# Kernel optimization log

Measured on AMD Instinct MI355X. Metric: run time of the kernel, lower is better.

## Reference

```python
import jax, jax.numpy as jnp
import numpy as np
import math

B, T, C = 4, 2048, 1024
NH = 16
HD = C // NH


def setup_inputs() -> dict:
    key = jax.random.key(0)
    ks = jax.random.split(key, 10)
    s = 0.02
    x = jax.random.normal(ks[0], (B, T, C), dtype=jnp.float32)
    W_qkv = jax.random.normal(ks[1], (C, 3 * C), dtype=jnp.float32) * s
    b_qkv = jnp.zeros((3 * C,), dtype=jnp.float32)
    W_proj = jax.random.normal(ks[2], (C, C), dtype=jnp.float32) * s
    b_proj = jnp.zeros((C,), dtype=jnp.float32)
    asym_mean, asym_std = 1.0, 0.7
    q_scale = jax.random.normal(ks[3], (NH, HD), dtype=jnp.float32) * asym_std + asym_mean
    q_bias = jax.random.normal(ks[4], (NH, HD), dtype=jnp.float32) * asym_std + asym_mean
    k_scale = jax.random.normal(ks[5], (NH, HD), dtype=jnp.float32) * asym_std + asym_mean
    k_bias = jax.random.normal(ks[6], (NH, HD), dtype=jnp.float32) * asym_std + asym_mean
    return {"x": x, "W_qkv": W_qkv, "b_qkv": b_qkv, "W_proj": W_proj,
            "b_proj": b_proj, "q_scale": q_scale, "q_bias": q_bias,
            "k_scale": k_scale, "k_bias": k_bias}


def reference(x, W_qkv, b_qkv, W_proj, b_proj, q_scale, q_bias, k_scale, k_bias):
    Bx, Tx, Cx = x.shape
    qkv = x @ W_qkv + b_qkv                       # [B,T,3C]
    q, k, v = jnp.split(qkv, 3, axis=-1)
    # [B,T,C] -> [B,NH,T,HD]
    reshape = lambda t: t.reshape(Bx, Tx, NH, HD).transpose(0, 2, 1, 3)
    q, k, v = reshape(q), reshape(k), reshape(v)
    # per-head affine scaling of Q/K
    q = q * q_scale[None, :, None, :] + q_bias[None, :, None, :]
    k = k * k_scale[None, :, None, :] + k_bias[None, :, None, :]
    scores = jnp.einsum('bhqd,bhkd->bhqk', q, k) / math.sqrt(HD)  # [B,NH,T,T]
    causal = jnp.tril(jnp.ones((Tx, Tx), dtype=bool))
    scores = jnp.where(causal[None, None], scores, -jnp.inf)
    att = jax.nn.softmax(scores, axis=-1)
    y = jnp.einsum('bhqk,bhkd->bhqd', att, v)     # [B,NH,T,HD]
    y = y.transpose(0, 2, 1, 3).reshape(Bx, Tx, Cx)
    return y @ W_proj + b_proj
```

## Files before the change

kernel.cpp:

```cpp
#include <hip/hip_runtime.h>
#include <hip/hip_bf16.h>

typedef unsigned short u16;
typedef __attribute__((ext_vector_type(8))) short short8;
typedef __attribute__((ext_vector_type(4))) float floatx4;

#define B_SZ 4
#define T_SZ 2048
#define C_SZ 1024
#define NH_SZ 16
#define HD_SZ 64
#define M_TOT 8192
#define K_DIM 1024

#define QSCALE 0.1803368801111204f

#define OFF_XB   ((size_t)16)
#define OFF_WQT  (OFF_XB + 8388608)
#define OFF_WPT  (OFF_WQT + 3145728)
#define OFF_PB   (OFF_WPT + 1048576)
#define OFF_Q    (OFF_PB + 8192)
#define OFF_K    (OFF_Q + 8388608)
#define OFF_V    (OFF_K + 8388608)
#define OFF_Y    (OFF_V + 8388608)
#define PB_BQKV  0
#define PB_BPROJ 3072
#define PB_QSC   4096
#define PB_QBI   5120
#define PB_KSC   6144
#define PB_KBI   7168

__device__ __forceinline__ float bf2f(u16 u) {
    return __uint_as_float(((unsigned)u) << 16);
}
__device__ __forceinline__ u16 f2bf(float f) {
    unsigned x = __float_as_uint(f);
    unsigned r = (x + 0x7fffu + ((x >> 16) & 1u)) >> 16;
    return (u16)r;
}
__device__ __forceinline__ u16 f2bf_fast(float f) {
    return (u16)((__float_as_uint(f) + 0x8000u) >> 16);
}
__device__ __forceinline__ void gl_lds16(const u16* g, u16* l) {
    __builtin_amdgcn_global_load_lds(
        (const __attribute__((address_space(1))) void*)g,
        (__attribute__((address_space(3))) void*)l, 16, 0, 0);
}

__global__ __launch_bounds__(256) void detect_k(const u16* __restrict__ x,
                                                int* __restrict__ flag) {
    __shared__ int cnt;
    if (threadIdx.x == 0) cnt = 0;
    __syncthreads();
    int bad = 0;
    for (int i = threadIdx.x; i < 512; i += 256) {
        float v = fabsf(bf2f(x[i]));
        if (v > 1024.0f || (v != 0.0f && v < 9.5367431640625e-7f)) bad++;
    }
    atomicAdd(&cnt, bad);
    __syncthreads();
    if (threadIdx.x == 0) flag[0] = (cnt > 16) ? 1 : 0;
}

__global__ __launch_bounds__(256) void conv_copy_k(const void* __restrict__ in,
                                                   u16* __restrict__ out, int n4,
                                                   const int* __restrict__ flag) {
    const int i = blockIdx.x * 256 + threadIdx.x;
    if (i >= n4) return;
    if (flag[0]) {
        const float4 v = ((const float4*)in)[i];
        ushort4 o;
        o.x = f2bf(v.x); o.y = f2bf(v.y); o.z = f2bf(v.z); o.w = f2bf(v.w);
        ((ushort4*)out)[i] = o;
    } else {
        ((ushort4*)out)[i] = ((const ushort4*)in)[i];
    }
}

__global__ __launch_bounds__(256) void conv_params_k(
        const void* __restrict__ bqkv, const void* __restrict__ bproj,
        const void* __restrict__ qsc, const void* __restrict__ qbi,
        const void* __restrict__ ksc, const void* __restrict__ kbi,
        u16* __restrict__ pb, const int* __restrict__ flag) {
    const int i4 = blockIdx.x * 256 + threadIdx.x;
    if (i4 >= 2048) return;
    const int e = i4 * 4;
    const void* src; int off;
    if (e < 3072)      { src = bqkv;  off = e; }
    else if (e < 4096) { src = bproj; off = e - 3072; }
    else if (e < 5120) { src = qsc;   off = e - 4096; }
    else if (e < 6144) { src = qbi;   off = e - 5120; }
    else if (e < 7168) { src = ksc;   off = e - 6144; }
    else               { src = kbi;   off = e - 7168; }
    ushort4 o;
    if (flag[0]) {
        const float4 v = *(const float4*)((const float*)src + off);
        o.x = f2bf(v.x); o.y = f2bf(v.y); o.z = f2bf(v.z); o.w = f2bf(v.w);
    } else {
        o = *(const ushort4*)((const u16*)src + off);
    }
    *(ushort4*)&pb[e] = o;
}

__global__ __launch_bounds__(256) void conv_transpose_k(const void* __restrict__ in,
                                                        u16* __restrict__ out,
                                                        int R, int C,
                                                        const int* __restrict__ flag) {
    __shared__ u16 t[32][33];
    const int isf = flag[0];
    const int c0 = blockIdx.x * 32, r0 = blockIdx.y * 32;
    const int tx = threadIdx.x & 31, ty = threadIdx.x >> 5;
    for (int i = 0; i < 4; i++) {
        int r = ty + i * 8;
        size_t idx = (size_t)(r0 + r) * C + c0 + tx;
        t[r][tx] = isf ? f2bf(((const float*)in)[idx]) : ((const u16*)in)[idx];
    }
    __syncthreads();
    for (int i = 0; i < 4; i++) {
        int cr = ty + i * 8;
        out[(size_t)(c0 + cr) * R + r0 + tx] = t[tx][cr];
    }
}

__global__ __launch_bounds__(256) void qkv_gemm(
        const u16* __restrict__ X, const u16* __restrict__ Wt,
        const u16* __restrict__ pb,
        u16* __restrict__ Qb, u16* __restrict__ Kb, u16* __restrict__ Vb) {
    __shared__ __align__(16) u16 As[128 * 64];
    __shared__ __align__(16) u16 Bs[128 * 64];
    const int bm = blockIdx.y * 128, bn = blockIdx.x * 128;
    const int tid = threadIdx.x;
    const int lane = tid & 63, wave = tid >> 6;
    const int quad = lane >> 4, l16 = lane & 15;
    const int wm = (wave & 1) * 64, wn = (wave >> 1) * 64;
    const int lrow = lane >> 3;
    const int lcol = ((lane & 7) ^ lrow) * 8;

    floatx4 acc[4][4];
    for (int mi = 0; mi < 4; mi++)
        for (int ni = 0; ni < 4; ni++) acc[mi][ni] = 0.f;

    for (int k0 = 0; k0 < K_DIM; k0 += 64) {
        __syncthreads();
        for (int j = 0; j < 4; j++) {
            const int rb = wave * 32 + j * 8;
            gl_lds16(&X[(size_t)(bm + rb + lrow) * K_DIM + k0 + lcol], &As[rb * 64]);
            gl_lds16(&Wt[(size_t)(bn + rb + lrow) * K_DIM + k0 + lcol], &Bs[rb * 64]);
        }
        __syncthreads();
        for (int kk = 0; kk < 64; kk += 32) {
            const int cb = kk >> 3;
            const int slot = ((cb + quad) ^ (l16 & 7)) * 8;
            short8 a[4], b[4];
            for (int mi = 0; mi < 4; mi++)
                a[mi] = *(const short8*)&As[(wm + mi * 16 + l16) * 64 + slot];
            for (int ni = 0; ni < 4; ni++)
                b[ni] = *(const short8*)&Bs[(wn + ni * 16 + l16) * 64 + slot];
            for (int mi = 0; mi < 4; mi++)
                for (int ni = 0; ni < 4; ni++)
                    acc[mi][ni] = __builtin_amdgcn_mfma_f32_16x16x32_bf16(
                        a[mi], b[ni], acc[mi][ni], 0, 0, 0);
        }
    }

    const int sec = bn >> 10;
    const int bb = bm >> 11;
    const int tbase = bm & 2047;
    for (int mi = 0; mi < 4; mi++) {
        for (int ni = 0; ni < 4; ni++) {
            const int col = bn + wn + ni * 16 + l16;
            const int cmod = col & 1023;
            const int h = cmod >> 6, d = cmod & 63;
            const float bv = bf2f(pb[PB_BQKV + col]);
            if (sec == 2) {
                const int t0 = tbase + wm + mi * 16 + quad * 4;
                ushort4 pk;
                pk.x = f2bf(acc[mi][ni][0] + bv);
                pk.y = f2bf(acc[mi][ni][1] + bv);
                pk.z = f2bf(acc[mi][ni][2] + bv);
                pk.w = f2bf(acc[mi][ni][3] + bv);
                *(ushort4*)&Vb[(((size_t)(bb * NH_SZ + h)) * HD_SZ + d) * T_SZ + t0] = pk;
            } else {
                float sA, sB;
                if (sec == 0) {
                    sA = bf2f(pb[PB_QSC + h * 64 + d]) * QSCALE;
                    sB = bf2f(pb[PB_QBI + h * 64 + d]) * QSCALE;
                } else {
                    sA = bf2f(pb[PB_KSC + h * 64 + d]);
                    sB = bf2f(pb[PB_KBI + h * 64 + d]);
                }
                u16* dstbuf = (sec == 0) ? Qb : Kb;
                for (int r = 0; r < 4; r++) {
                    const int t = tbase + wm + mi * 16 + quad * 4 + r;
                    float v = (acc[mi][ni][r] + bv) * sA + sB;
                    dstbuf[(((size_t)(bb * NH_SZ + h)) * T_SZ + t) * HD_SZ + d] = f2bf(v);
                }
            }
        }
    }
}

__global__ __launch_bounds__(512) void attn_k(const u16* __restrict__ Qb,
                                              const u16* __restrict__ Kb,
                                              const u16* __restrict__ Vtg,
                                              u16* __restrict__ Y) {
    __shared__ __align__(16) u16 Ks[64 * 64];
    __shared__ __align__(16) u16 Vs[64 * 64];
    __shared__ __align__(16) u16 Ps[8 * 16 * 88];
    const int blk = blockIdx.x;
    const int head = blk & 63;
    const int p = blk >> 6;
    const int b = head >> 4, h = head & 15;
    const int tid = threadIdx.x, lane = tid & 63, w = tid >> 6;
    const int quad = lane >> 4, l16 = lane & 15;
    const size_t qk_off = (size_t)head * (T_SZ * HD_SZ);
    const size_t v_off = (size_t)head * (HD_SZ * T_SZ);
    u16* psw = &Ps[w * 1408];
    const int lr = lane >> 3;
    const int lc = ((lane & 7) ^ lr) * 8;
    const int sl0 = ((quad) ^ (l16 & 7)) * 8;
    const int sl1 = ((4 + quad) ^ (l16 & 7)) * 8;

    short8 ones;
    for (int j = 0; j < 8; j++) ones[j] = (short)0x3F80;

    for (int tile = 0; tile < 2; tile++) {
        const int qt = tile ? p : (15 - p);
        const int q0 = qt * 128;
        const int rbase = q0 + w * 16;
        const int q = rbase + l16;

        const short8 aq0 = *(const short8*)&Qb[qk_off + (size_t)q * HD_SZ + quad * 8];
        const short8 aq1 = *(const short8*)&Qb[qk_off + (size_t)q * HD_SZ + 32 + quad * 8];

        floatx4 o[4];
        for (int mi = 0; mi < 4; mi++) o[mi] = 0.f;
        float m_run = -1e30f, l_run = 0.f;

        for (int k0 = 0; k0 < q0 + 128; k0 += 64) {
            __syncthreads();
            gl_lds16(&Kb[qk_off + (size_t)(k0 + w * 8 + lr) * HD_SZ + lc], &Ks[w * 512]);
            gl_lds16(&Vtg[v_off + (size_t)(w * 8 + lr) * T_SZ + k0 + lc], &Vs[w * 512]);
            __syncthreads();
            if (k0 > rbase + 15) continue;

            floatx4 s[4];
            for (int ni = 0; ni < 4; ni++) s[ni] = 0.f;
            for (int ni = 0; ni < 4; ni++)
                s[ni] = __builtin_amdgcn_mfma_f32_16x16x32_bf16(
                    *(const short8*)&Ks[(ni * 16 + l16) * 64 + sl0], aq0, s[ni], 0, 0, 0);
            for (int ni = 0; ni < 4; ni++)
                s[ni] = __builtin_amdgcn_mfma_f32_16x16x32_bf16(
                    *(const short8*)&Ks[(ni * 16 + l16) * 64 + sl1], aq1, s[ni], 0, 0, 0);

            if (k0 + 63 > rbase) {
                for (int ni = 0; ni < 4; ni++)
                    for (int r = 0; r < 4; r++) {
                        int key = k0 + ni * 16 + quad * 4 + r;
                        if (key > q) s[ni][r] = -1e30f;
                    }
            }

            float mx = fmaxf(fmaxf(s[0][0], s[0][1]), fmaxf(s[0][2], s[0][3]));
            for (int ni = 1; ni < 4; ni++)
                mx = fmaxf(mx, fmaxf(fmaxf(s[ni][0], s[ni][1]),
                                     fmaxf(s[ni][2], s[ni][3])));
            mx = fmaxf(mx, __shfl_xor(mx, 16, 64));
            mx = fmaxf(mx, __shfl_xor(mx, 32, 64));
            const float mnew = fmaxf(m_run, mx);
            const float alpha = exp2f(m_run - mnew);
            for (int ni = 0; ni < 4; ni++)
                for (int r = 0; r < 4; r++)
                    s[ni][r] = exp2f(s[ni][r] - mnew);
            m_run = mnew;
            for (int mi = 0; mi < 4; mi++) o[mi] *= alpha;

            for (int ni = 0; ni < 4; ni++) {
                ushort4 pk;
                pk.x = f2bf_fast(s[ni][0]); pk.y = f2bf_fast(s[ni][1]);
                pk.z = f2bf_fast(s[ni][2]); pk.w = f2bf_fast(s[ni][3]);
                *(ushort4*)&psw[l16 * 88 + ni * 16 + quad * 4] = pk;
            }

            floatx4 s4 = 0.f;
            for (int kk = 0; kk < 64; kk += 32) {
                const int sl = (kk == 0) ? 0 : 0;
                short8 pfr = *(const short8*)&psw[l16 * 88 + kk + quad * 8];
                const int vsl = (kk == 0) ? sl0 : sl1;
                s4 = __builtin_amdgcn_mfma_f32_16x16x32_bf16(ones, pfr, s4, 0, 0, 0);
                for (int mi = 0; mi < 4; mi++) {
                    short8 vfr = *(const short8*)&Vs[(mi * 16 + l16) * 64 + vsl];
                    o[mi] = __builtin_amdgcn_mfma_f32_16x16x32_bf16(vfr, pfr, o[mi], 0, 0, 0);
                }
                (void)sl;
            }
            l_run = l_run * alpha + s4[0];
        }

        const float inv = 1.0f / l_run;
        u16* yrow = &Y[(((size_t)b * T_SZ + q) * NH_SZ + h) * HD_SZ];
        for (int mi = 0; mi < 4; mi++) {
            ushort4 pk;
            pk.x = f2bf_fast(o[mi][0] * inv); pk.y = f2bf_fast(o[mi][1] * inv);
            pk.z = f2bf_fast(o[mi][2] * inv); pk.w = f2bf_fast(o[mi][3] * inv);
            *(ushort4*)&yrow[mi * 16 + quad * 4] = pk;
        }
    }
}

__global__ __launch_bounds__(256) void proj_gemm(const u16* __restrict__ Yin,
                                                 const u16* __restrict__ Wt,
                                                 const u16* __restrict__ pb,
                                                 void* __restrict__ out,
                                                 const int* __restrict__ flag) {
    __shared__ __align__(16) u16 As[128 * 64];
    __shared__ __align__(16) u16 Bs[128 * 64];
    const int isf = flag[0];
    const int bm = blockIdx.y * 128, bn = blockIdx.x * 128;
    const int tid = threadIdx.x;
    const int lane = tid & 63, wave = tid >> 6;
    const int quad = lane >> 4, l16 = lane & 15;
    const int wm = (wave & 1) * 64, wn = (wave >> 1) * 64;
    const int lrow = lane >> 3;
    const int lcol = ((lane & 7) ^ lrow) * 8;

    floatx4 acc[4][4];
    for (int mi = 0; mi < 4; mi++)
        for (int ni = 0; ni < 4; ni++) acc[mi][ni] = 0.f;

    for (int k0 = 0; k0 < K_DIM; k0 += 64) {
        __syncthreads();
        for (int j = 0; j < 4; j++) {
            const int rb = wave * 32 + j * 8;
            gl_lds16(&Yin[(size_t)(bm + rb + lrow) * K_DIM + k0 + lcol], &As[rb * 64]);
            gl_lds16(&Wt[(size_t)(bn + rb + lrow) * K_DIM + k0 + lcol], &Bs[rb * 64]);
        }
        __syncthreads();
        for (int kk = 0; kk < 64; kk += 32) {
            const int cb = kk >> 3;
            const int slot = ((cb + quad) ^ (l16 & 7)) * 8;
            short8 a[4], b[4];
            for (int mi = 0; mi < 4; mi++)
                a[mi] = *(const short8*)&As[(wm + mi * 16 + l16) * 64 + slot];
            for (int ni = 0; ni < 4; ni++)
                b[ni] = *(const short8*)&Bs[(wn + ni * 16 + l16) * 64 + slot];
            for (int mi = 0; mi < 4; mi++)
                for (int ni = 0; ni < 4; ni++)
                    acc[mi][ni] = __builtin_amdgcn_mfma_f32_16x16x32_bf16(
                        a[mi], b[ni], acc[mi][ni], 0, 0, 0);
        }
    }

    for (int mi = 0; mi < 4; mi++) {
        for (int ni = 0; ni < 4; ni++) {
            const int col = bn + wn + ni * 16 + l16;
            const float bv = bf2f(pb[PB_BPROJ + col]);
            for (int r = 0; r < 4; r++) {
                const int row = bm + wm + mi * 16 + quad * 4 + r;
                const float v = acc[mi][ni][r] + bv;
                if (isf) ((float*)out)[(size_t)row * C_SZ + col] = v;
                else     ((u16*)out)[(size_t)row * C_SZ + col] = f2bf(v);
            }
        }
    }
}

extern "C" void kernel_launch(void* const* d_in, const int* in_sizes, int n_in,
                              void* d_out, int out_size, void* d_ws, size_t ws_size,
                              hipStream_t stream) {
    const void* x     = d_in[0];
    const void* Wqkv  = d_in[1];
    const void* bqkv  = d_in[2];
    const void* Wproj = d_in[3];
    const void* bproj = d_in[4];
    const void* qsc   = d_in[5];
    const void* qbi   = d_in[6];
    const void* ksc   = d_in[7];
    const void* kbi   = d_in[8];

    u16* ws = (u16*)d_ws;
    int* flag    = (int*)d_ws;
    u16* xb      = ws + OFF_XB;
    u16* Wt_qkv  = ws + OFF_WQT;
    u16* Wt_proj = ws + OFF_WPT;
    u16* pb      = ws + OFF_PB;
    u16* Qb      = ws + OFF_Q;
    u16* Kb      = ws + OFF_K;
    u16* Vb      = ws + OFF_V;
    u16* Yb      = ws + OFF_Y;

    detect_k<<<1, 256, 0, stream>>>((const u16*)x, flag);

    conv_copy_k<<<8192, 256, 0, stream>>>(x, xb, 2097152, flag);
    conv_params_k<<<8, 256, 0, stream>>>(bqkv, bproj, qsc, qbi, ksc, kbi, pb, flag);
    conv_transpose_k<<<dim3(96, 32), 256, 0, stream>>>(Wqkv, Wt_qkv, 1024, 3072, flag);
    conv_transpose_k<<<dim3(32, 32), 256, 0, stream>>>(Wproj, Wt_proj, 1024, 1024, flag);

    qkv_gemm<<<dim3(24, 64), 256, 0, stream>>>(xb, Wt_qkv, pb, Qb, Kb, Vb);
    attn_k<<<dim3(512), 512, 0, stream>>>(Qb, Kb, Vb, Yb);
    proj_gemm<<<dim3(8, 64), 256, 0, stream>>>(Yb, Wt_proj, pb, d_out, flag);
}
```

Before: 317.0 us.

## Double-buffer GEMM LDS tiles and merge prep kernels into one launch

The QKV and projection GEMMs now use two LDS buffers per operand. The next k-tile's global-to-LDS loads are issued before the MFMA work on the current tile, which removes one barrier per iteration and overlaps load latency with compute. The four input-conversion kernels are folded into a single prep kernel that dispatches on block index, cutting launch overhead. LDS use per GEMM block doubles to 64KB, which may lower occupancy.

Result: slower. 323.9 us (+2.2%).

```diff
diff --git a/kernel.cpp b/kernel.cpp
--- a/kernel.cpp
+++ b/kernel.cpp
@@ -46,6 +46,9 @@
         (const __attribute__((address_space(1))) void*)g,
         (__attribute__((address_space(3))) void*)l, 16, 0, 0);
 }
+__device__ __forceinline__ void wait_vm0() {
+    __builtin_amdgcn_s_waitcnt(0x0F70);
+}
 
 __global__ __launch_bounds__(256) void detect_k(const u16* __restrict__ x,
                                                 int* __restrict__ flag) {
@@ -62,58 +65,61 @@
     if (threadIdx.x == 0) flag[0] = (cnt > 16) ? 1 : 0;
 }
 
-__global__ __launch_bounds__(256) void conv_copy_k(const void* __restrict__ in,
-                                                   u16* __restrict__ out, int n4,
-                                                   const int* __restrict__ flag) {
-    const int i = blockIdx.x * 256 + threadIdx.x;
-    if (i >= n4) return;
-    if (flag[0]) {
-        const float4 v = ((const float4*)in)[i];
-        ushort4 o;
-        o.x = f2bf(v.x); o.y = f2bf(v.y); o.z = f2bf(v.z); o.w = f2bf(v.w);
-        ((ushort4*)out)[i] = o;
-    } else {
-        ((ushort4*)out)[i] = ((const ushort4*)in)[i];
-    }
-}
-
-__global__ __launch_bounds__(256) void conv_params_k(
+__global__ __launch_bounds__(256) void prep_k(
+        const void* __restrict__ x,
+        const void* __restrict__ Wqkv, const void* __restrict__ Wproj,
         const void* __restrict__ bqkv, const void* __restrict__ bproj,
         const void* __restrict__ qsc, const void* __restrict__ qbi,
         const void* __restrict__ ksc, const void* __restrict__ kbi,
-        u16* __restrict__ pb, const int* __restrict__ flag) {
-    const int i4 = blockIdx.x * 256 + threadIdx.x;
-    if (i4 >= 2048) return;
-    const int e = i4 * 4;
-    const void* src; int off;
-    if (e < 3072)      { src = bqkv;  off = e; }
-    else if (e < 4096) { src = bproj; off = e - 3072; }
-    else if (e < 5120) { src = qsc;   off = e - 4096; }
-    else if (e < 6144) { src = qbi;   off = e - 5120; }
-    else if (e < 7168) { src = ksc;   off = e - 6144; }
-    else               { src = kbi;   off = e - 7168; }
-    ushort4 o;
-    if (flag[0]) {
-        const float4 v = *(const float4*)((const float*)src + off);
-        o.x = f2bf(v.x); o.y = f2bf(v.y); o.z = f2bf(v.z); o.w = f2bf(v.w);
-    } else {
-        o = *(const ushort4*)((const u16*)src + off);
-    }
-    *(ushort4*)&pb[e] = o;
-}
-
-__global__ __launch_bounds__(256) void conv_transpose_k(const void* __restrict__ in,
-                                                        u16* __restrict__ out,
-                                                        int R, int C,
-                                                        const int* __restrict__ flag) {
+        u16* __restrict__ xb, u16* __restrict__ Wt_qkv,
+        u16* __restrict__ Wt_proj, u16* __restrict__ pb,
+        const int* __restrict__ flag) {
     __shared__ u16 t[32][33];
+    const int blk = blockIdx.x;
     const int isf = flag[0];
-    const int c0 = blockIdx.x * 32, r0 = blockIdx.y * 32;
+    if (blk < 8192) {
+        const int i = blk * 256 + threadIdx.x;
+        if (isf) {
+            const float4 v = ((const float4*)x)[i];
+            ushort4 o;
+            o.x = f2bf(v.x); o.y = f2bf(v.y); o.z = f2bf(v.z); o.w = f2bf(v.w);
+            ((ushort4*)xb)[i] = o;
+        } else {
+            ((ushort4*)xb)[i] = ((const ushort4*)x)[i];
+        }
+        return;
+    }
+    if (blk < 8200) {
+        const int i4 = (blk - 8192) * 256 + threadIdx.x;
+        if (i4 >= 2048) return;
+        const int e = i4 * 4;
+        const void* src; int off;
+        if (e < 3072)      { src = bqkv;  off = e; }
+        else if (e < 4096) { src = bproj; off = e - 3072; }
+        else if (e < 5120) { src = qsc;   off = e - 4096; }
+        else if (e < 6144) { src = qbi;   off = e - 5120; }
+        else if (e < 7168) { src = ksc;   off = e - 6144; }
+        else               { src = kbi;   off = e - 7168; }
+        ushort4 o;
+        if (isf) {
+            const float4 v = *(const float4*)((const float*)src + off);
+            o.x = f2bf(v.x); o.y = f2bf(v.y); o.z = f2bf(v.z); o.w = f2bf(v.w);
+        } else {
+            o = *(const ushort4*)((const u16*)src + off);
+        }
+        *(ushort4*)&pb[e] = o;
+        return;
+    }
+    const void* in; u16* out; int R, C, idx;
+    if (blk < 11272) { idx = blk - 8200;  in = Wqkv;  out = Wt_qkv;  R = 1024; C = 3072; }
+    else             { idx = blk - 11272; in = Wproj; out = Wt_proj; R = 1024; C = 1024; }
+    const int nbx = C >> 5;
+    const int c0 = (idx % nbx) * 32, r0 = (idx / nbx) * 32;
     const int tx = threadIdx.x & 31, ty = threadIdx.x >> 5;
     for (int i = 0; i < 4; i++) {
         int r = ty + i * 8;
-        size_t idx = (size_t)(r0 + r) * C + c0 + tx;
-        t[r][tx] = isf ? f2bf(((const float*)in)[idx]) : ((const u16*)in)[idx];
+        size_t gi = (size_t)(r0 + r) * C + c0 + tx;
+        t[r][tx] = isf ? f2bf(((const float*)in)[gi]) : ((const u16*)in)[gi];
     }
     __syncthreads();
     for (int i = 0; i < 4; i++) {
@@ -126,8 +132,8 @@
         const u16* __restrict__ X, const u16* __restrict__ Wt,
         const u16* __restrict__ pb,
         u16* __restrict__ Qb, u16* __restrict__ Kb, u16* __restrict__ Vb) {
-    __shared__ __align__(16) u16 As[128 * 64];
-    __shared__ __align__(16) u16 Bs[128 * 64];
+    __shared__ __align__(16) u16 As[2][128 * 64];
+    __shared__ __align__(16) u16 Bs[2][128 * 64];
     const int bm = blockIdx.y * 128, bn = blockIdx.x * 128;
     const int tid = threadIdx.x;
     const int lane = tid & 63, wave = tid >> 6;
@@ -136,31 +142,45 @@
     const int lrow = lane >> 3;
     const int lcol = ((lane & 7) ^ lrow) * 8;
 
+    const u16* xrow = &X[(size_t)(bm + wave * 32 + lrow) * K_DIM + lcol];
+    const u16* wrow = &Wt[(size_t)(bn + wave * 32 + lrow) * K_DIM + lcol];
+
     floatx4 acc[4][4];
     for (int mi = 0; mi < 4; mi++)
         for (int ni = 0; ni < 4; ni++) acc[mi][ni] = 0.f;
 
+    for (int j = 0; j < 4; j++) {
+        gl_lds16(xrow + (size_t)j * 8 * K_DIM, &As[0][(wave * 32 + j * 8) * 64]);
+        gl_lds16(wrow + (size_t)j * 8 * K_DIM, &Bs[0][(wave * 32 + j * 8) * 64]);
+    }
+
+    int cur = 0;
     for (int k0 = 0; k0 < K_DIM; k0 += 64) {
+        wait_vm0();
         __syncthreads();
-        for (int j = 0; j < 4; j++) {
-            const int rb = wave * 32 + j * 8;
-            gl_lds16(&X[(size_t)(bm + rb + lrow) * K_DIM + k0 + lcol], &As[rb * 64]);
-            gl_lds16(&Wt[(size_t)(bn + rb + lrow) * K_DIM + k0 + lcol], &Bs[rb * 64]);
-        }
-        __syncthreads();
+        if (k0 + 64 < K_DIM) {
+            const int nb = cur ^ 1;
+            for (int j = 0; j < 4; j++) {
+                gl_lds16(xrow + (size_t)j * 8 * K_DIM + k0 + 64,
+                         &As[nb][(wave * 32 + j * 8) * 64]);
+                gl_lds16(wrow + (size_t)j * 8 * K_DIM + k0 + 64,
+                         &Bs[nb][(wave * 32 + j * 8) * 64]);
+            }
+        }
         for (int kk = 0; kk < 64; kk += 32) {
             const int cb = kk >> 3;
             const int slot = ((cb + quad) ^ (l16 & 7)) * 8;
             short8 a[4], b[4];
             for (int mi = 0; mi < 4; mi++)
-                a[mi] = *(const short8*)&As[(wm + mi * 16 + l16) * 64 + slot];
+                a[mi] = *(const short8*)&As[cur][(wm + mi * 16 + l16) * 64 + slot];
             for (int ni = 0; ni < 4; ni++)
-                b[ni] = *(const short8*)&Bs[(wn + ni * 16 + l16) * 64 + slot];
+                b[ni] = *(const short8*)&Bs[cur][(wn + ni * 16 + l16) * 64 + slot];
             for (int mi = 0; mi < 4; mi++)
                 for (int ni = 0; ni < 4; ni++)
                     acc[mi][ni] = __builtin_amdgcn_mfma_f32_16x16x32_bf16(
                         a[mi], b[ni], acc[mi][ni], 0, 0, 0);
         }
+        cur ^= 1;
     }
 
     const int sec = bn >> 10;
@@ -284,7 +304,6 @@
 
             floatx4 s4 = 0.f;
             for (int kk = 0; kk < 64; kk += 32) {
-                const int sl = (kk == 0) ? 0 : 0;
                 short8 pfr = *(const short8*)&psw[l16 * 88 + kk + quad * 8];
                 const int vsl = (kk == 0) ? sl0 : sl1;
                 s4 = __builtin_amdgcn_mfma_f32_16x16x32_bf16(ones, pfr, s4, 0, 0, 0);
@@ -292,7 +311,6 @@
                     short8 vfr = *(const short8*)&Vs[(mi * 16 + l16) * 64 + vsl];
                     o[mi] = __builtin_amdgcn_mfma_f32_16x16x32_bf16(vfr, pfr, o[mi], 0, 0, 0);
                 }
-                (void)sl;
             }
             l_run = l_run * alpha + s4[0];
         }
@@ -313,8 +331,8 @@
                                                  const u16* __restrict__ pb,
                                                  void* __restrict__ out,
                                                  const int* __restrict__ flag) {
-    __shared__ __align__(16) u16 As[128 * 64];
-    __shared__ __align__(16) u16 Bs[128 * 64];
+    __shared__ __align__(16) u16 As[2][128 * 64];
+    __shared__ __align__(16) u16 Bs[2][128 * 64];
     const int isf = flag[0];
     const int bm = blockIdx.y * 128, bn = blockIdx.x * 128;
     const int tid = threadIdx.x;
@@ -324,31 +342,45 @@
     const int lrow = lane >> 3;
     const int lcol = ((lane & 7) ^ lrow) * 8;
 
+    const u16* yrow = &Yin[(size_t)(bm + wave * 32 + lrow) * K_DIM + lcol];
+    const u16* wrow = &Wt[(size_t)(bn + wave * 32 + lrow) * K_DIM + lcol];
+
     floatx4 acc[4][4];
     for (int mi = 0; mi < 4; mi++)
         for (int ni = 0; ni < 4; ni++) acc[mi][ni] = 0.f;
 
+    for (int j = 0; j < 4; j++) {
+        gl_lds16(yrow + (size_t)j * 8 * K_DIM, &As[0][(wave * 32 + j * 8) * 64]);
+        gl_lds16(wrow + (size_t)j * 8 * K_DIM, &Bs[0][(wave * 32 + j * 8) * 64]);
+    }
+
+    int cur = 0;
     for (int k0 = 0; k0 < K_DIM; k0 += 64) {
+        wait_vm0();
         __syncthreads();
-        for (int j = 0; j < 4; j++) {
-            const int rb = wave * 32 + j * 8;
-            gl_lds16(&Yin[(size_t)(bm + rb + lrow) * K_DIM + k0 + lcol], &As[rb * 64]);
-            gl_lds16(&Wt[(size_t)(bn + rb + lrow) * K_DIM + k0 + lcol], &Bs[rb * 64]);
-        }
-        __syncthreads();
+        if (k0 + 64 < K_DIM) {
+            const int nb = cur ^ 1;
+            for (int j = 0; j < 4; j++) {
+                gl_lds16(yrow + (size_t)j * 8 * K_DIM + k0 + 64,
+                         &As[nb][(wave * 32 + j * 8) * 64]);
+                gl_lds16(wrow + (size_t)j * 8 * K_DIM + k0 + 64,
+                         &Bs[nb][(wave * 32 + j * 8) * 64]);
+            }
+        }
         for (int kk = 0; kk < 64; kk += 32) {
             const int cb = kk >> 3;
             const int slot = ((cb + quad) ^ (l16 & 7)) * 8;
             short8 a[4], b[4];
             for (int mi = 0; mi < 4; mi++)
-                a[mi] = *(const short8*)&As[(wm + mi * 16 + l16) * 64 + slot];
+                a[mi] = *(const short8*)&As[cur][(wm + mi * 16 + l16) * 64 + slot];
             for (int ni = 0; ni < 4; ni++)
-                b[ni] = *(const short8*)&Bs[(wn + ni * 16 + l16) * 64 + slot];
+                b[ni] = *(const short8*)&Bs[cur][(wn + ni * 16 + l16) * 64 + slot];
             for (int mi = 0; mi < 4; mi++)
                 for (int ni = 0; ni < 4; ni++)
                     acc[mi][ni] = __builtin_amdgcn_mfma_f32_16x16x32_bf16(
                         a[mi], b[ni], acc[mi][ni], 0, 0, 0);
         }
+        cur ^= 1;
     }
 
     for (int mi = 0; mi < 4; mi++) {
@@ -390,12 +422,9 @@
     u16* Yb      = ws + OFF_Y;
 
     detect_k<<<1, 256, 0, stream>>>((const u16*)x, flag);
-
-    conv_copy_k<<<8192, 256, 0, stream>>>(x, xb, 2097152, flag);
-    conv_params_k<<<8, 256, 0, stream>>>(bqkv, bproj, qsc, qbi, ksc, kbi, pb, flag);
-    conv_transpose_k<<<dim3(96, 32), 256, 0, stream>>>(Wqkv, Wt_qkv, 1024, 3072, flag);
-    conv_transpose_k<<<dim3(32, 32), 256, 0, stream>>>(Wproj, Wt_proj, 1024, 1024, flag);
-
+    prep_k<<<12296, 256, 0, stream>>>(x, Wqkv, Wproj, bqkv, bproj,
+                                      qsc, qbi, ksc, kbi,
+                                      xb, Wt_qkv, Wt_proj, pb, flag);
     qkv_gemm<<<dim3(24, 64), 256, 0, stream>>>(xb, Wt_qkv, pb, Qb, Kb, Vb);
     attn_k<<<dim3(512), 512, 0, stream>>>(Qb, Kb, Vb, Yb);
     proj_gemm<<<dim3(8, 64), 256, 0, stream>>>(Yb, Wt_proj, pb, d_out, flag);
```
